# Kernel optimization log

Hardware: AMD Instinct MI355X
Metric: run time of the kernel (lower is better)

The kernel has to match this reference:

```python
import jax, jax.numpy as jnp
import numpy as np

B, T, D, H = 4, 2048, 1024, 16
HD = D // H  # 64
LOCAL_CTX, BLOCKSIZE, VERTSIZE = 256, 1, 16
STRIDE = LOCAL_CTX // BLOCKSIZE  # 256


def build_fixed_mask(n):
    # num_verts == 1 branch of generate_fixed_attention_mask
    layout = np.zeros((n, n), dtype=np.bool_)
    # vertical stripes: top `vertsize` indices of each stride block
    for idx in range(STRIDE - VERTSIZE, STRIDE):
        layout[:, idx::STRIDE] = True
    rows = np.arange(n)
    # local: each query attends to its own stride-block
    same_block = (rows[:, None] // STRIDE) == (rows[None, :] // STRIDE)
    layout |= same_block
    # causal: zero out k > q
    layout &= rows[None, :] <= rows[:, None]
    return layout


def setup_inputs() -> dict:
    key = jax.random.key(0)
    k1, k2, k3, k4, k5 = jax.random.split(key, 5)
    s = 0.02
    return {
        "x": jax.random.normal(k1, (B, T, D), dtype=jnp.float32),
        "Wqkv": jax.random.normal(k2, (D, 3 * D), dtype=jnp.float32) * s,
        "bqkv": jax.random.normal(k3, (3 * D,), dtype=jnp.float32) * s,
        "Wproj": jax.random.normal(k4, (D, D), dtype=jnp.float32) * s,
        "bproj": jax.random.normal(k5, (D,), dtype=jnp.float32) * s,
        "mask": jnp.asarray(build_fixed_mask(T)),
    }


def reference(x, Wqkv, bqkv, Wproj, bproj, mask):
    b, t, _ = x.shape
    qkv = (x @ Wqkv + bqkv).reshape(b, t, 3, H, HD)
    # (B,T,3,H,HD) -> (B,H,T,HD) per component
    q = qkv[:, :, 0].transpose(0, 2, 1, 3)
    k = qkv[:, :, 1].transpose(0, 2, 1, 3)
    v = qkv[:, :, 2].transpose(0, 2, 1, 3)
    att = jnp.einsum("bhqd,bhkd->bhqk", q, k) * (1.0 / jnp.sqrt(jnp.float32(HD)))
    att = jnp.where(mask[:t, :t], att, -jnp.inf)
    att = jax.nn.softmax(att, axis=-1)
    y = jnp.einsum("bhqk,bhkd->bhqd", att, v)
    y = y.transpose(0, 2, 1, 3).reshape(b, t, D)
    return y @ Wproj + bproj
```

## Files before the change

### kernel.cpp

```cpp
#include <hip/hip_runtime.h>
#include <cstdint>
#include <cstddef>

typedef unsigned short u16;
typedef __attribute__((ext_vector_type(8))) short short8;
typedef __attribute__((ext_vector_type(4))) float f32x4;
typedef __attribute__((ext_vector_type(4))) unsigned short u16x4;

#define B_ 4
#define T_ 2048
#define D_ 1024
#define H_ 16
#define HD_ 64

__device__ __forceinline__ u16 f2bf(float f) {
  union { float f; unsigned i; } v; v.f = f;
  unsigned r = (v.i + 0x7FFFu + ((v.i >> 16) & 1u)) >> 16;
  return (u16)r;
}

__device__ __forceinline__ void load_lds16(const void* g, void* l) {
  __builtin_amdgcn_global_load_lds(
      (const __attribute__((address_space(1))) void*)g,
      (__attribute__((address_space(3))) void*)l, 16, 0, 0);
}

__global__ __launch_bounds__(256) void cvt_f32_bf16(const float* __restrict__ src,
                                                    u16* __restrict__ dst) {
  const size_t i = ((size_t)blockIdx.x * 256 + threadIdx.x) * 4;
  const f32x4 v = *(const f32x4*)(src + i);
  u16x4 o;
#pragma unroll
  for (int r = 0; r < 4; ++r) o[r] = f2bf(v[r]);
  *(u16x4*)(dst + i) = o;
}

__global__ __launch_bounds__(256) void transpose_cvt(const float* __restrict__ src,
                                                     u16* __restrict__ dst,
                                                     int R, int C) {
  __shared__ u16 t[32][33];
  const int c0 = blockIdx.x * 32, r0 = blockIdx.y * 32;
  const int tid = threadIdx.x;
  const int lr = tid >> 5, lc = tid & 31;
#pragma unroll
  for (int p = 0; p < 4; ++p)
    t[lr + p * 8][lc] = f2bf(src[(size_t)(r0 + lr + p * 8) * C + c0 + lc]);
  __syncthreads();
#pragma unroll
  for (int p = 0; p < 4; ++p)
    dst[(size_t)(c0 + lr + p * 8) * R + r0 + lc] = t[lc][lr + p * 8];
}

template <int EPI>
__global__ __launch_bounds__(256)
void gemm_bt(const u16* __restrict__ A, const u16* __restrict__ Bt,
             const float* __restrict__ bias, int K, int N,
             void* __restrict__ o0v, u16* __restrict__ o1, u16* __restrict__ o2) {
  __shared__ u16 As[128 * 32];
  __shared__ u16 Bs[128 * 32];
  const int tid = threadIdx.x;
  const int lane = tid & 63;
  const int w = tid >> 6;
  const int q = lane >> 4, col = lane & 15;
  const int m0 = blockIdx.y * 128, n0 = blockIdx.x * 128;
  const int wm = (w >> 1) * 64, wn = (w & 1) * 64;
  const int srow = tid >> 2;
  const int soff = (((tid & 3) ^ ((srow >> 1) & 3)) * 8);
  const int slot = (q ^ ((col >> 1) & 3)) * 8;

  f32x4 acc[4][4] = {};

  const u16* Ap = A + (size_t)(m0 + srow) * K + soff;
  const u16* Bp = Bt + (size_t)(n0 + srow) * K + soff;

  for (int kb = 0; kb < K; kb += 32) {
    load_lds16(Ap + kb, &As[tid * 8]);
    load_lds16(Ap + (size_t)64 * K + kb, &As[2048 + tid * 8]);
    load_lds16(Bp + kb, &Bs[tid * 8]);
    load_lds16(Bp + (size_t)64 * K + kb, &Bs[2048 + tid * 8]);
    __syncthreads();
    short8 af[4], bfr[4];
#pragma unroll
    for (int i = 0; i < 4; ++i)
      af[i] = *(const short8*)&As[(wm + i * 16 + col) * 32 + slot];
#pragma unroll
    for (int j = 0; j < 4; ++j)
      bfr[j] = *(const short8*)&Bs[(wn + j * 16 + col) * 32 + slot];
#pragma unroll
    for (int i = 0; i < 4; ++i)
#pragma unroll
      for (int j = 0; j < 4; ++j)
        acc[i][j] = __builtin_amdgcn_mfma_f32_16x16x32_bf16(af[i], bfr[j], acc[i][j], 0, 0, 0);
    __syncthreads();
  }

#pragma unroll
  for (int j = 0; j < 4; ++j) {
    const int n = n0 + wn + j * 16 + col;
    const float bv = bias[n];
    if constexpr (EPI == 0) {
      u16* q0p = (u16*)o0v;
      const int c = n >> 10, rem = n & 1023, hh = rem >> 6, dd = rem & 63;
#pragma unroll
      for (int i = 0; i < 4; ++i) {
        const int mrow = m0 + wm + i * 16 + q * 4;
        const int b = mrow >> 11, t = mrow & 2047;
        const int bh = b * H_ + hh;
        if (c == 0) {
#pragma unroll
          for (int r = 0; r < 4; ++r)
            q0p[((size_t)bh * T_ + t + r) * HD_ + dd] = f2bf((acc[i][j][r] + bv) * 0.125f);
        } else if (c == 1) {
#pragma unroll
          for (int r = 0; r < 4; ++r)
            o1[((size_t)bh * T_ + t + r) * HD_ + dd] = f2bf(acc[i][j][r] + bv);
        } else {
          u16x4 pk;
#pragma unroll
          for (int r = 0; r < 4; ++r) pk[r] = f2bf(acc[i][j][r] + bv);
          *(u16x4*)&o2[((size_t)bh * HD_ + dd) * T_ + t] = pk;
        }
      }
    } else {
      float* outp = (float*)o0v;
#pragma unroll
      for (int i = 0; i < 4; ++i) {
        const int mrow = m0 + wm + i * 16 + q * 4;
#pragma unroll
        for (int r = 0; r < 4; ++r)
          outp[(size_t)(mrow + r) * N + n] = acc[i][j][r] + bv;
      }
    }
  }
}

__global__ __launch_bounds__(256)
void sparse_attn(const u16* __restrict__ Qb, const u16* __restrict__ Kb,
                 const u16* __restrict__ Vt, u16* __restrict__ Y) {
  __shared__ char smem[20480];
  u16* Pall = (u16*)smem;
  float* Obuf = (float*)smem;

  const int tid = threadIdx.x, lane = tid & 63, w = tid >> 6;
  const int q = lane >> 4, col = lane & 15;
  const int bh = blockIdx.y, qt = blockIdx.x;
  const int b = bh >> 4, hh = bh & 15;
  const int qb = qt >> 2;
  const int rb = (qt & 3) * 64;
  const int qg = qt * 64;
  const u16* Qh = Qb + (size_t)bh * T_ * HD_;
  const u16* Kh = Kb + (size_t)bh * T_ * HD_;
  const u16* Vh = Vt + (size_t)bh * HD_ * T_;

  short8 qf[4][2];
#pragma unroll
  for (int i = 0; i < 4; ++i)
#pragma unroll
    for (int h2 = 0; h2 < 2; ++h2)
      qf[i][h2] = *(const short8*)&Qh[(size_t)(qg + i * 16 + col) * HD_ + h2 * 32 + q * 8];

  f32x4 o[4][4] = {};
  f32x4 lI[4] = {};
  const short8 ones = {0x3F80, 0x3F80, 0x3F80, 0x3F80, 0x3F80, 0x3F80, 0x3F80, 0x3F80};

  u16* P = Pall + w * 2560;

  const int ns = (qb + 1) >> 1;
  const int L = ns + 2 * (qt & 3) + 2;

  for (int j = w; j < L; j += 4) {
    int k0, k1, localc;
    bool mask1;
    if (j < ns) {
      k0 = (2 * j) * 256 + 240; k1 = k0 + 256;
      mask1 = (2 * j + 1 == qb); localc = -1;
    } else {
      const int c = j - ns;
      k0 = qb * 256 + c * 32; k1 = k0 + 16;
      mask1 = false; localc = c * 32;
    }
    short8 k0a = *(const short8*)&Kh[(size_t)(k0 + col) * HD_ + q * 8];
    short8 k0b = *(const short8*)&Kh[(size_t)(k0 + col) * HD_ + 32 + q * 8];
    short8 k1a = *(const short8*)&Kh[(size_t)(k1 + col) * HD_ + q * 8];
    short8 k1b = *(const short8*)&Kh[(size_t)(k1 + col) * HD_ + 32 + q * 8];
#pragma unroll
    for (int rt = 0; rt < 4; ++rt) {
      f32x4 z = {0.f, 0.f, 0.f, 0.f};
      f32x4 s0 = __builtin_amdgcn_mfma_f32_16x16x32_bf16(qf[rt][0], k0a, z, 0, 0, 0);
      s0 = __builtin_amdgcn_mfma_f32_16x16x32_bf16(qf[rt][1], k0b, s0, 0, 0, 0);
      f32x4 s1 = __builtin_amdgcn_mfma_f32_16x16x32_bf16(qf[rt][0], k1a, z, 0, 0, 0);
      s1 = __builtin_amdgcn_mfma_f32_16x16x32_bf16(qf[rt][1], k1b, s1, 0, 0, 0);
#pragma unroll
      for (int r = 0; r < 4; ++r) {
        float p0 = __expf(s0[r]);
        float p1 = mask1 ? 0.f : __expf(s1[r]);
        if (localc >= 0) {
          const int qr = rb + rt * 16 + q * 4 + r;
          if (localc + col > qr) p0 = 0.f;
          if (localc + 16 + col > qr) p1 = 0.f;
        }
        P[(rt * 16 + q * 4 + r) * 40 + col] = f2bf(p0);
        P[(rt * 16 + q * 4 + r) * 40 + 16 + col] = f2bf(p1);
      }
    }
    asm volatile("s_waitcnt lgkmcnt(0)" ::: "memory");
    short8 pf[4], vf[4];
#pragma unroll
    for (int rt = 0; rt < 4; ++rt)
      pf[rt] = *(const short8*)&P[(rt * 16 + col) * 40 + q * 8];
    const int kvb = (q < 2) ? (k0 + q * 8) : (k1 + (q - 2) * 8);
#pragma unroll
    for (int dt = 0; dt < 4; ++dt)
      vf[dt] = *(const short8*)&Vh[(size_t)(dt * 16 + col) * T_ + kvb];
#pragma unroll
    for (int rt = 0; rt < 4; ++rt) {
#pragma unroll
      for (int dt = 0; dt < 4; ++dt)
        o[rt][dt] = __builtin_amdgcn_mfma_f32_16x16x32_bf16(pf[rt], vf[dt], o[rt][dt], 0, 0, 0);
      lI[rt] = __builtin_amdgcn_mfma_f32_16x16x32_bf16(pf[rt], ones, lI[rt], 0, 0, 0);
    }
  }

#pragma unroll
  for (int rt = 0; rt < 4; ++rt) {
    __syncthreads();
#pragma unroll
    for (int dt = 0; dt < 4; ++dt)
      *(f32x4*)&Obuf[(w * 65 + dt * 16 + col) * 16 + q * 4] = o[rt][dt];
    if (col == 0)
      *(f32x4*)&Obuf[(w * 65 + 64) * 16 + q * 4] = lI[rt];
    __syncthreads();
    f32x4 acc = {0.f, 0.f, 0.f, 0.f};
    f32x4 lt = {0.f, 0.f, 0.f, 0.f};
#pragma unroll
    for (int w2 = 0; w2 < 4; ++w2) {
      acc += *(const f32x4*)&Obuf[(w2 * 65 + w * 16 + col) * 16 + q * 4];
      lt += *(const f32x4*)&Obuf[(w2 * 65 + 64) * 16 + q * 4];
    }
#pragma unroll
    for (int r = 0; r < 4; ++r) {
      const int trow = qg + rt * 16 + q * 4 + r;
      Y[((size_t)(b * T_ + trow)) * D_ + hh * HD_ + w * 16 + col] = f2bf(acc[r] / lt[r]);
    }
  }
}

extern "C" void kernel_launch(void* const* d_in, const int* in_sizes, int n_in,
                              void* d_out, int out_size, void* d_ws, size_t ws_size,
                              hipStream_t stream) {
  const float* x = (const float*)d_in[0];
  const float* Wqkv = (const float*)d_in[1];
  const float* bqkv = (const float*)d_in[2];
  const float* Wproj = (const float*)d_in[3];
  const float* bproj = (const float*)d_in[4];
  float* out = (float*)d_out;

  char* ws = (char*)d_ws;
  u16* xb     = (u16*)(ws + 0);
  u16* WqkvT  = (u16*)(ws + 16777216);
  u16* WprojT = (u16*)(ws + 23068672);
  u16* Qb     = (u16*)(ws + 25165824);
  u16* Kb     = (u16*)(ws + 41943040);
  u16* Vt     = (u16*)(ws + 58720256);
  u16* Y      = (u16*)(ws + 75497472);

  cvt_f32_bf16<<<dim3(8192), 256, 0, stream>>>(x, xb);
  transpose_cvt<<<dim3(96, 32), 256, 0, stream>>>(Wqkv, WqkvT, 1024, 3072);
  transpose_cvt<<<dim3(32, 32), 256, 0, stream>>>(Wproj, WprojT, 1024, 1024);
  gemm_bt<0><<<dim3(24, 64), 256, 0, stream>>>(xb, WqkvT, bqkv, 1024, 3072, Qb, Kb, Vt);
  sparse_attn<<<dim3(32, 64), 256, 0, stream>>>(Qb, Kb, Vt, Y);
  gemm_bt<1><<<dim3(8, 64), 256, 0, stream>>>(Y, WprojT, bproj, 1024, 1024, out, nullptr, nullptr);
}
```

Baseline: 272.0 us.

## Restructure sparse attention to per-wave query rows with blocked V layout

The V tensor is now stored in 16-key blocks (T/16 x HD x 16) instead of a plain transpose. The attention kernel assigns each wave its own 16 query rows and iterates over 16-key chunks, computing S^T so P stays in registers and feeds the PV MFMA directly. This removes the LDS round-trip for P, the cross-wave reduction through shared memory, and the __syncthreads. Block order is reversed so the heaviest query tiles launch first. In exchange, half of each PV MFMA's K dimension is zero padding, and waves within a block now carry uneven loop counts.

```diff
diff --git a/kernel.cpp b/kernel.cpp
--- a/kernel.cpp
+++ b/kernel.cpp
@@ -118,7 +118,8 @@
           u16x4 pk;
 #pragma unroll
           for (int r = 0; r < 4; ++r) pk[r] = f2bf(acc[i][j][r] + bv);
-          *(u16x4*)&o2[((size_t)bh * HD_ + dd) * T_ + t] = pk;
+          *(u16x4*)&o2[(size_t)bh * (T_ * HD_) + (size_t)(t >> 4) * (HD_ * 16) +
+                       dd * 16 + (t & 15)] = pk;
         }
       }
     } else {
@@ -137,111 +138,63 @@
 __global__ __launch_bounds__(256)
 void sparse_attn(const u16* __restrict__ Qb, const u16* __restrict__ Kb,
                  const u16* __restrict__ Vt, u16* __restrict__ Y) {
-  __shared__ char smem[20480];
-  u16* Pall = (u16*)smem;
-  float* Obuf = (float*)smem;
-
-  const int tid = threadIdx.x, lane = tid & 63, w = tid >> 6;
-  const int q = lane >> 4, col = lane & 15;
-  const int bh = blockIdx.y, qt = blockIdx.x;
+  const int tid = threadIdx.x, lane = tid & 63, wv = tid >> 6;
+  const int cq = lane & 15, qd = lane >> 4;
+  const int bh = blockIdx.y;
+  const int qt = 31 - blockIdx.x;
   const int b = bh >> 4, hh = bh & 15;
   const int qb = qt >> 2;
-  const int rb = (qt & 3) * 64;
-  const int qg = qt * 64;
+  const int qg = qt * 64 + wv * 16;
   const u16* Qh = Qb + (size_t)bh * T_ * HD_;
   const u16* Kh = Kb + (size_t)bh * T_ * HD_;
-  const u16* Vh = Vt + (size_t)bh * HD_ * T_;
-
-  short8 qf[4][2];
-#pragma unroll
-  for (int i = 0; i < 4; ++i)
-#pragma unroll
-    for (int h2 = 0; h2 < 2; ++h2)
-      qf[i][h2] = *(const short8*)&Qh[(size_t)(qg + i * 16 + col) * HD_ + h2 * 32 + q * 8];
-
-  f32x4 o[4][4] = {};
-  f32x4 lI[4] = {};
-  const short8 ones = {0x3F80, 0x3F80, 0x3F80, 0x3F80, 0x3F80, 0x3F80, 0x3F80, 0x3F80};
-
-  u16* P = Pall + w * 2560;
-
-  const int ns = (qb + 1) >> 1;
-  const int L = ns + 2 * (qt & 3) + 2;
-
-  for (int j = w; j < L; j += 4) {
-    int k0, k1, localc;
-    bool mask1;
-    if (j < ns) {
-      k0 = (2 * j) * 256 + 240; k1 = k0 + 256;
-      mask1 = (2 * j + 1 == qb); localc = -1;
-    } else {
-      const int c = j - ns;
-      k0 = qb * 256 + c * 32; k1 = k0 + 16;
-      mask1 = false; localc = c * 32;
+  const u16* Vh = Vt + (size_t)bh * T_ * HD_;
+
+  const short8 qf0 = *(const short8*)&Qh[(size_t)(qg + cq) * HD_ + qd * 8];
+  const short8 qf1 = *(const short8*)&Qh[(size_t)(qg + cq) * HD_ + 32 + qd * 8];
+
+  f32x4 o[4] = {};
+  float lsum = 0.f;
+
+  const int nloc = (qt & 3) * 4 + wv + 1;
+  const int L = qb + nloc;
+
+  for (int j = 0; j < L; ++j) {
+    const int kb = (j < qb) ? (j * 256 + 240) : (qb * 256 + (j - qb) * 16);
+    const bool diag = (j == L - 1);
+    const short8 ka = *(const short8*)&Kh[(size_t)(kb + cq) * HD_ + qd * 8];
+    const short8 kb8 = *(const short8*)&Kh[(size_t)(kb + cq) * HD_ + 32 + qd * 8];
+    const u16* vblk = Vh + (size_t)(kb >> 4) * (HD_ * 16);
+    short8 vf[4];
+#pragma unroll
+    for (int dt = 0; dt < 4; ++dt) {
+      const u16x4 vv = *(const u16x4*)&vblk[(dt * 16 + cq) * 16 + qd * 4];
+      vf[dt] = short8{(short)vv[0], (short)vv[1], (short)vv[2], (short)vv[3], 0, 0, 0, 0};
     }
-    short8 k0a = *(const short8*)&Kh[(size_t)(k0 + col) * HD_ + q * 8];
-    short8 k0b = *(const short8*)&Kh[(size_t)(k0 + col) * HD_ + 32 + q * 8];
-    short8 k1a = *(const short8*)&Kh[(size_t)(k1 + col) * HD_ + q * 8];
-    short8 k1b = *(const short8*)&Kh[(size_t)(k1 + col) * HD_ + 32 + q * 8];
-#pragma unroll
-    for (int rt = 0; rt < 4; ++rt) {
-      f32x4 z = {0.f, 0.f, 0.f, 0.f};
-      f32x4 s0 = __builtin_amdgcn_mfma_f32_16x16x32_bf16(qf[rt][0], k0a, z, 0, 0, 0);
-      s0 = __builtin_amdgcn_mfma_f32_16x16x32_bf16(qf[rt][1], k0b, s0, 0, 0, 0);
-      f32x4 s1 = __builtin_amdgcn_mfma_f32_16x16x32_bf16(qf[rt][0], k1a, z, 0, 0, 0);
-      s1 = __builtin_amdgcn_mfma_f32_16x16x32_bf16(qf[rt][1], k1b, s1, 0, 0, 0);
-#pragma unroll
-      for (int r = 0; r < 4; ++r) {
-        float p0 = __expf(s0[r]);
-        float p1 = mask1 ? 0.f : __expf(s1[r]);
-        if (localc >= 0) {
-          const int qr = rb + rt * 16 + q * 4 + r;
-          if (localc + col > qr) p0 = 0.f;
-          if (localc + 16 + col > qr) p1 = 0.f;
-        }
-        P[(rt * 16 + q * 4 + r) * 40 + col] = f2bf(p0);
-        P[(rt * 16 + q * 4 + r) * 40 + 16 + col] = f2bf(p1);
-      }
+    const f32x4 z = {0.f, 0.f, 0.f, 0.f};
+    f32x4 s = __builtin_amdgcn_mfma_f32_16x16x32_bf16(ka, qf0, z, 0, 0, 0);
+    s = __builtin_amdgcn_mfma_f32_16x16x32_bf16(kb8, qf1, s, 0, 0, 0);
+    short8 p = {0, 0, 0, 0, 0, 0, 0, 0};
+#pragma unroll
+    for (int r = 0; r < 4; ++r) {
+      float e = __expf(s[r]);
+      if (diag && (qd * 4 + r) > cq) e = 0.f;
+      lsum += e;
+      p[r] = (short)f2bf(e);
     }
-    asm volatile("s_waitcnt lgkmcnt(0)" ::: "memory");
-    short8 pf[4], vf[4];
-#pragma unroll
-    for (int rt = 0; rt < 4; ++rt)
-      pf[rt] = *(const short8*)&P[(rt * 16 + col) * 40 + q * 8];
-    const int kvb = (q < 2) ? (k0 + q * 8) : (k1 + (q - 2) * 8);
 #pragma unroll
     for (int dt = 0; dt < 4; ++dt)
-      vf[dt] = *(const short8*)&Vh[(size_t)(dt * 16 + col) * T_ + kvb];
-#pragma unroll
-    for (int rt = 0; rt < 4; ++rt) {
-#pragma unroll
-      for (int dt = 0; dt < 4; ++dt)
-        o[rt][dt] = __builtin_amdgcn_mfma_f32_16x16x32_bf16(pf[rt], vf[dt], o[rt][dt], 0, 0, 0);
-      lI[rt] = __builtin_amdgcn_mfma_f32_16x16x32_bf16(pf[rt], ones, lI[rt], 0, 0, 0);
-    }
-  }
-
-#pragma unroll
-  for (int rt = 0; rt < 4; ++rt) {
-    __syncthreads();
-#pragma unroll
-    for (int dt = 0; dt < 4; ++dt)
-      *(f32x4*)&Obuf[(w * 65 + dt * 16 + col) * 16 + q * 4] = o[rt][dt];
-    if (col == 0)
-      *(f32x4*)&Obuf[(w * 65 + 64) * 16 + q * 4] = lI[rt];
-    __syncthreads();
-    f32x4 acc = {0.f, 0.f, 0.f, 0.f};
-    f32x4 lt = {0.f, 0.f, 0.f, 0.f};
-#pragma unroll
-    for (int w2 = 0; w2 < 4; ++w2) {
-      acc += *(const f32x4*)&Obuf[(w2 * 65 + w * 16 + col) * 16 + q * 4];
-      lt += *(const f32x4*)&Obuf[(w2 * 65 + 64) * 16 + q * 4];
-    }
-#pragma unroll
-    for (int r = 0; r < 4; ++r) {
-      const int trow = qg + rt * 16 + q * 4 + r;
-      Y[((size_t)(b * T_ + trow)) * D_ + hh * HD_ + w * 16 + col] = f2bf(acc[r] / lt[r]);
-    }
+      o[dt] = __builtin_amdgcn_mfma_f32_16x16x32_bf16(vf[dt], p, o[dt], 0, 0, 0);
+  }
+
+  float lt = lsum + __shfl_xor(lsum, 16);
+  lt += __shfl_xor(lt, 32);
+  const float inv = 1.0f / lt;
+#pragma unroll
+  for (int dt = 0; dt < 4; ++dt) {
+    u16x4 pk;
+#pragma unroll
+    for (int r = 0; r < 4; ++r) pk[r] = f2bf(o[dt][r] * inv);
+    *(u16x4*)&Y[((size_t)(b * T_ + qg + cq)) * D_ + hh * HD_ + dt * 16 + qd * 4] = pk;
   }
 }
 
```

After: 286.1 us. +5.2%, slower.
